# Kernel optimization log

Measured on AMD Instinct MI355X. Metric: run time of the kernel, lower is better.

The kernel has to match this reference:

```python
import jax, jax.numpy as jnp
import numpy as np
from functools import partial

N_NODES = 100000
N_REL = 3
N_EDGES = 200000
IN_F = 128
HID_F = 128
OUT_F = 128
N_QUERY = 4096


def _graph_conv(x, es, ed, W, b, n_nodes):
    """DGL GraphConv with norm='both': D_dst^{-1/2} A D_src^{-1/2} X W + b.
    es/ed: [E] int edge endpoints, x: [N, d_in], W: [d_in, d_out], b: [d_out]."""
    ones = jnp.ones(es.shape[0], dtype=x.dtype)
    out_deg = jnp.clip(jax.ops.segment_sum(ones, es, num_segments=n_nodes), 1.0)
    in_deg = jnp.clip(jax.ops.segment_sum(ones, ed, num_segments=n_nodes), 1.0)
    # transform first (dense GEMM), then gather -> scatter-add over dst
    y = (x * jax.lax.rsqrt(out_deg)[:, None]) @ W          # [N, d_out]
    msg = y[es]                                            # [E, d_out] gather
    agg = jax.ops.segment_sum(msg, ed, num_segments=n_nodes)  # [N, d_out]
    return agg * jax.lax.rsqrt(in_deg)[:, None] + b


def _hetero_layer(x, e_src, e_dst, W, b, n_nodes):
    # HeteroGraphConv(aggregate='sum'): sum per-relation GraphConv outputs.
    out = _graph_conv(x, e_src[0], e_dst[0], W[0], b[0], n_nodes)
    for r in range(1, e_src.shape[0]):
        out = out + _graph_conv(x, e_src[r], e_dst[r], W[r], b[r], n_nodes)
    return out


def setup_inputs() -> dict:
    key = jax.random.key(0)
    ks = jax.random.split(key, 9)
    s = 1.0 / np.sqrt(IN_F)
    return {
        "emb": jax.random.normal(ks[0], (N_NODES, IN_F), jnp.float32),
        "W1": jax.random.normal(ks[1], (N_REL, IN_F, HID_F), jnp.float32) * s,
        "b1": jnp.zeros((N_REL, HID_F), jnp.float32),
        "W2": jax.random.normal(ks[2], (N_REL, HID_F, OUT_F), jnp.float32) * s,
        "b2": jnp.zeros((N_REL, OUT_F), jnp.float32),
        "e_src": jax.random.randint(ks[3], (N_REL, N_EDGES), 0, N_NODES, jnp.int32),
        "e_dst": jax.random.randint(ks[4], (N_REL, N_EDGES), 0, N_NODES, jnp.int32),
        "src": jax.random.randint(ks[5], (N_QUERY,), 0, N_NODES, jnp.int32),
        "dst": jax.random.randint(ks[6], (N_QUERY,), 0, N_NODES, jnp.int32),
    }


def reference(emb, W1, b1, W2, b2, e_src, e_dst, src, dst):
    n = emb.shape[0]
    h = jnp.tanh(_hetero_layer(emb, e_src, e_dst, W1, b1, n))
    h = jnp.tanh(_hetero_layer(h, e_src, e_dst, W2, b2, n))
    return (h[src], h[dst])
```

## Files before the change

### kernel.cpp

```cpp
#include <hip/hip_runtime.h>
#include <stdint.h>

#define NN 100000
#define NREL 3
#define NE 200000
#define F 128
#define NQ 4096

#define NBUCK (NREL * NN)
#define NCB ((NBUCK + 255) / 256)
#define CH_BLOCKS 512
#define CH_CHUNK ((NREL * NE + CH_BLOCKS - 1) / CH_BLOCKS)

#define WCVT_N (2 * NREL * F * F)
#define A1 (WCVT_N + 256)
#define A2 (A1 + NN * F / 8)
#define A3 (A2 + 2 * NQ)
#define A4 (A3 + NN)
#define PREP_N (A4 + 1)

typedef float fx4 __attribute__((ext_vector_type(4)));
typedef unsigned short u16x8 __attribute__((ext_vector_type(8)));
typedef __bf16 bf16x8 __attribute__((ext_vector_type(8)));

__device__ __forceinline__ unsigned short f2bf(float f) {
  uint32_t u = __builtin_bit_cast(uint32_t, f);
  uint32_t r = u + 0x7FFFu + ((u >> 16) & 1u);
  return (unsigned short)(r >> 16);
}
__device__ __forceinline__ float bf2f(unsigned short u) {
  return __builtin_bit_cast(float, (uint32_t)u << 16);
}
__device__ __forceinline__ int rel_of(int i) {
  return (i >= 2 * NE) ? 2 : (i >= NE ? 1 : 0);
}

__global__ void prep_kernel(const float* __restrict__ W1, const float* __restrict__ W2,
                            const float* __restrict__ b1, const float* __restrict__ b2,
                            const float* __restrict__ emb,
                            const int* __restrict__ qsrc, const int* __restrict__ qdst,
                            unsigned short* __restrict__ Wtb, float* __restrict__ bsum,
                            unsigned short* __restrict__ xb,
                            int* __restrict__ qnode, int* __restrict__ mark,
                            int* __restrict__ cursor) {
  int i = blockIdx.x * blockDim.x + threadIdx.x;
  if (i < WCVT_N) {
    int l = i / (NREL * F * F);
    int rem = i % (NREL * F * F);
    int r = rem / (F * F);
    int nk = rem % (F * F);
    int n = nk >> 7, k = nk & 127;
    const float* W = l ? W2 : W1;
    Wtb[i] = f2bf(W[r * F * F + k * F + n]);
  } else if (i < A1) {
    int t = i - WCVT_N;
    int l = t >> 7, f = t & 127;
    const float* b = l ? b2 : b1;
    bsum[l * F + f] = b[f] + b[F + f] + b[2 * F + f];
  } else if (i < A2) {
    int j = i - A1;
    const float* p = emb + (size_t)j * 8;
    unsigned short tmp[8];
#pragma unroll
    for (int e = 0; e < 8; ++e) tmp[e] = f2bf(p[e]);
    *reinterpret_cast<u16x8*>(xb + (size_t)j * 8) = *reinterpret_cast<u16x8*>(tmp);
  } else if (i < A3) {
    int m = i - A2;
    qnode[m] = (m < NQ) ? qsrc[m] : qdst[m - NQ];
  } else if (i < A4) {
    mark[i - A3] = 0;
  } else if (i < PREP_N) {
    *cursor = 0;
  }
}

__global__ __launch_bounds__(256) void coarseHH_kernel(const int* __restrict__ es,
                                                       const int* __restrict__ ed,
                                                       int* __restrict__ Hd,
                                                       int* __restrict__ Hs) {
  __shared__ int hd[NCB], hs[NCB];
  int t = threadIdx.x, blk = blockIdx.x;
  for (int j = t; j < NCB; j += 256) { hd[j] = 0; hs[j] = 0; }
  __syncthreads();
  int lo = blk * CH_CHUNK;
  int hi = min(lo + CH_CHUNK, NREL * NE);
  for (int i = lo + t; i < hi; i += 256) {
    int r = rel_of(i);
    atomicAdd(&hd[(r * NN + ed[i]) >> 8], 1);
    atomicAdd(&hs[(r * NN + es[i]) >> 8], 1);
  }
  __syncthreads();
  for (int j = t; j < NCB; j += 256) {
    Hd[j * CH_BLOCKS + blk] = hd[j];
    Hs[j * CH_BLOCKS + blk] = hs[j];
  }
}

__global__ __launch_bounds__(256) void hsum_kernel(const int* __restrict__ Hd,
                                                   const int* __restrict__ Hs,
                                                   int* __restrict__ chist_d,
                                                   int* __restrict__ chist_s) {
  int t = threadIdx.x, lane = t & 63;
  int ws = blockIdx.x * 4 + (t >> 6);
  if (ws >= 2 * NCB) return;
  const int* H = (ws < NCB) ? Hd : Hs;
  int bin = (ws < NCB) ? ws : ws - NCB;
  int s = 0;
#pragma unroll
  for (int k = 0; k < 8; ++k) s += H[bin * CH_BLOCKS + lane * 8 + k];
#pragma unroll
  for (int d = 1; d < 64; d <<= 1) s += __shfl_xor(s, d);
  if (lane == 0) {
    if (ws < NCB) chist_d[bin] = s; else chist_s[bin] = s;
  }
}

__global__ __launch_bounds__(256) void cscan_kernel(const int* __restrict__ chist_d,
                                                    const int* __restrict__ chist_s,
                                                    int* __restrict__ cstart_d,
                                                    int* __restrict__ cstart_s) {
  const int* chist = blockIdx.x ? chist_s : chist_d;
  int* cstart = blockIdx.x ? cstart_s : cstart_d;
  int t = threadIdx.x, lane = t & 63, w = t >> 6;
  int v[5];
  int s = 0;
#pragma unroll
  for (int k = 0; k < 5; ++k) {
    int i = t * 5 + k;
    v[k] = (i < NCB) ? chist[i] : 0;
    s += v[k];
  }
  int sc = s;
#pragma unroll
  for (int d = 1; d < 64; d <<= 1) {
    int o = __shfl_up(sc, d);
    if (lane >= d) sc += o;
  }
  __shared__ int wt[4];
  if (lane == 63) wt[w] = sc;
  __syncthreads();
  int woff = 0;
#pragma unroll
  for (int ww = 0; ww < 3; ++ww) woff += (ww < w) ? wt[ww] : 0;
  int excl = woff + sc - s;
#pragma unroll
  for (int k = 0; k < 5; ++k) {
    int i = t * 5 + k;
    if (i < NCB) { cstart[i] = excl; excl += v[k]; }
  }
}

__global__ __launch_bounds__(256) void hbase_kernel(const int* __restrict__ Hd,
                                                    const int* __restrict__ Hs,
                                                    const int* __restrict__ cstart_d,
                                                    const int* __restrict__ cstart_s,
                                                    int* __restrict__ Hbase_d,
                                                    int* __restrict__ Hbase_s) {
  const int* H = blockIdx.y ? Hs : Hd;
  const int* cstart = blockIdx.y ? cstart_s : cstart_d;
  int* Hbase = blockIdx.y ? Hbase_s : Hbase_d;
  int t = threadIdx.x, lane = t & 63;
  int bin = blockIdx.x * 4 + (t >> 6);
  int v[8];
  int s = 0;
#pragma unroll
  for (int k = 0; k < 8; ++k) {
    v[k] = H[bin * CH_BLOCKS + lane * 8 + k];
    s += v[k];
  }
  int sc = s;
#pragma unroll
  for (int d = 1; d < 64; d <<= 1) {
    int o = __shfl_up(sc, d);
    if (lane >= d) sc += o;
  }
  int run = cstart[bin] + sc - s;
#pragma unroll
  for (int k = 0; k < 8; ++k) {
    Hbase[bin * CH_BLOCKS + lane * 8 + k] = run;
    run += v[k];
  }
}

__global__ __launch_bounds__(256) void cscatter_kernel(const int* __restrict__ es,
                                                       const int* __restrict__ ed,
                                                       const int* __restrict__ Hbase_d,
                                                       const int* __restrict__ Hbase_s,
                                                       int* __restrict__ etmp_d,
                                                       int* __restrict__ etmp_s) {
  __shared__ int cur_d[NCB], cur_s[NCB];
  int t = threadIdx.x, blk = blockIdx.x;
  for (int j = t; j < NCB; j += 256) {
    cur_d[j] = Hbase_d[j * CH_BLOCKS + blk];
    cur_s[j] = Hbase_s[j * CH_BLOCKS + blk];
  }
  __syncthreads();
  int lo = blk * CH_CHUNK;
  int hi = min(lo + CH_CHUNK, NREL * NE);
  for (int i = lo + t; i < hi; i += 256) {
    int r = rel_of(i);
    int s = es[i], d = ed[i];
    int bd = r * NN + d;
    int pos = atomicAdd(&cur_d[bd >> 8], 1);
    etmp_d[pos] = (s << 8) | (bd & 255);
    int bs = r * NN + s;
    int pos_s = atomicAdd(&cur_s[bs >> 8], 1);
    etmp_s[pos_s] = bs & 255;
  }
}

__global__ __launch_bounds__(256) void srccount_kernel(const int* __restrict__ etmp_s,
                                                       const int* __restrict__ cstart_s,
                                                       const int* __restrict__ chist_s,
                                                       int* __restrict__ cnt_src) {
  const int cb = blockIdx.x;
  const int t = threadIdx.x;
  const int cs = cstart_s[cb], cc = chist_s[cb];
  __shared__ int fcnt[256];
  fcnt[t] = 0;
  __syncthreads();
  for (int i = t; i < cc; i += 256) atomicAdd(&fcnt[etmp_s[cs + i]], 1);
  __syncthreads();
  int b = cb * 256 + t;
  if (b < NBUCK) cnt_src[b] = fcnt[t];
}

__global__ __launch_bounds__(256) void fine_kernel(const int* __restrict__ etmp,
                                                   const int* __restrict__ cstart,
                                                   const int* __restrict__ chist,
                                                   const int* __restrict__ cnt_src,
                                                   int2* __restrict__ scb,
                                                   int2* __restrict__ epay) {
  const int cb = blockIdx.x;
  const int t = threadIdx.x, lane = t & 63, w = t >> 6;
  const int cs = cstart[cb], cc = chist[cb];
  __shared__ int fcnt[256], fexcl[256], fcur[256];
  fcnt[t] = 0;
  fcur[t] = 0;
  __syncthreads();
  for (int i = t; i < cc; i += 256) atomicAdd(&fcnt[etmp[cs + i] & 255], 1);
  __syncthreads();
  int val = fcnt[t];
  int sc = val;
#pragma unroll
  for (int d = 1; d < 64; d <<= 1) {
    int o = __shfl_up(sc, d);
    if (lane >= d) sc += o;
  }
  __shared__ int wt[4];
  if (lane == 63) wt[w] = sc;
  __syncthreads();
  int woff = 0;
#pragma unroll
  for (int ww = 0; ww < 3; ++ww) woff += (ww < w) ? wt[ww] : 0;
  fexcl[t] = woff + sc - val;
  int b = cb * 256 + t;
  if (b < NBUCK) scb[b] = make_int2(cs + fexcl[t], val);
  __syncthreads();
  for (int i = t; i < cc; i += 256) {
    int e = etmp[cs + i];
    int f = e & 255;
    int src = ((unsigned)e) >> 8;
    int r = (cb * 256 + f) / NN;
    float wgt = rsqrtf((float)cnt_src[r * NN + src]) * rsqrtf((float)fcnt[f]);
    int pos = cs + fexcl[f] + atomicAdd(&fcur[f], 1);
    epay[pos] = make_int2(src, __builtin_bit_cast(int, wgt));
  }
}

__global__ void mark_kernel(const int* __restrict__ qnode, const int2* __restrict__ scb,
                            const int2* __restrict__ epay, int* __restrict__ mark) {
  int m = blockIdx.x * blockDim.x + threadIdx.x;
  if (m >= 2 * NQ) return;
  int n = qnode[m];
#pragma unroll
  for (int r = 0; r < NREL; ++r) {
    int2 meta = scb[r * NN + n];
    for (int i = 0; i < meta.y; ++i) mark[epay[meta.x + i].x] = 1;
  }
}

__global__ __launch_bounds__(256) void compact_kernel(const int* __restrict__ mark,
                                                      int* __restrict__ list,
                                                      int* __restrict__ cursor) {
  int t = threadIdx.x, lane = t & 63, w = t >> 6;
  int base = blockIdx.x * 1024 + t * 4;
  int loc[4];
  int cnt = 0;
#pragma unroll
  for (int k = 0; k < 4; ++k) {
    int i = base + k;
    if (i < NN && mark[i]) { loc[cnt] = i; ++cnt; }
  }
  int sc = cnt;
#pragma unroll
  for (int d = 1; d < 64; d <<= 1) {
    int o = __shfl_up(sc, d);
    if (lane >= d) sc += o;
  }
  int texcl = sc - cnt;
  __shared__ int wt[4];
  __shared__ int bb;
  if (lane == 63) wt[w] = sc;
  __syncthreads();
  if (t == 0) {
    int tot = wt[0] + wt[1] + wt[2] + wt[3];
    bb = atomicAdd(cursor, tot);
    int a = 0;
#pragma unroll
    for (int ww = 0; ww < 4; ++ww) { int c = wt[ww]; wt[ww] = a; a += c; }
  }
  __syncthreads();
  int p = bb + wt[w] + texcl;
  for (int k = 0; k < cnt; ++k) list[p + k] = loc[k];
}

__global__ __launch_bounds__(256) void aggz_kernel(const unsigned short* __restrict__ X,
                                                   const int2* __restrict__ scb,
                                                   const int2* __restrict__ epay,
                                                   const int* __restrict__ nmap,
                                                   const int* __restrict__ cntp,
                                                   unsigned short* __restrict__ Z,
                                                   int Mcap, int Ms) {
  const int count = cntp ? *cntp : Mcap;
  const int r = blockIdx.y;
  const int t = threadIdx.x;
  const int lane = t & 63;
  const int m = blockIdx.x * 16 + (t >> 6) * 4 + (lane >> 4);
  const int j = lane & 15;
  if (m >= count) return;
  int n = nmap ? nmap[m] : m;
  int2 meta = scb[r * NN + n];
  const int2* ep = epay + meta.x;
  const int c = meta.y;

  float ps[8];
#pragma unroll
  for (int k = 0; k < 8; ++k) ps[k] = 0.f;

  int i = 0;
  for (; i + 2 <= c; i += 2) {
    int2 p0 = ep[i], p1 = ep[i + 1];
    float w0 = __builtin_bit_cast(float, p0.y);
    float w1 = __builtin_bit_cast(float, p1.y);
    u16x8 v0 = *reinterpret_cast<const u16x8*>(X + ((size_t)p0.x << 7) + j * 8);
    u16x8 v1 = *reinterpret_cast<const u16x8*>(X + ((size_t)p1.x << 7) + j * 8);
#pragma unroll
    for (int k = 0; k < 8; ++k)
      ps[k] = fmaf(bf2f(v1[k]), w1, fmaf(bf2f(v0[k]), w0, ps[k]));
  }
  if (i < c) {
    int2 p0 = ep[i];
    float w0 = __builtin_bit_cast(float, p0.y);
    u16x8 v0 = *reinterpret_cast<const u16x8*>(X + ((size_t)p0.x << 7) + j * 8);
#pragma unroll
    for (int k = 0; k < 8; ++k) ps[k] = fmaf(bf2f(v0[k]), w0, ps[k]);
  }

  unsigned short tmp[8];
#pragma unroll
  for (int k = 0; k < 8; ++k) tmp[k] = f2bf(ps[k]);
  *reinterpret_cast<u16x8*>(Z + (((size_t)r * Ms + m) << 7) + j * 8) =
      *reinterpret_cast<u16x8*>(tmp);
}

#define GBM 128
__global__ __launch_bounds__(512) void gemmp_kernel(const unsigned short* __restrict__ Z,
                                                    const unsigned short* __restrict__ Wt3,
                                                    const float* __restrict__ bsum,
                                                    const int* __restrict__ omap,
                                                    const int* __restrict__ cntp,
                                                    void* __restrict__ outp,
                                                    int M, int Ms, int out_f32) {
  const int count = cntp ? *cntp : M;
  const int m0 = blockIdx.x * GBM;
  if (m0 >= count) return;
  __shared__ unsigned short Abuf[2][GBM * F];
  const int t = threadIdx.x;
  const int lane = t & 63, w = t >> 6;
  const int wm = w >> 2, wn = w & 3;
  const int r0 = lane & 15, kq = lane >> 4;

  fx4 acc[4][2];
#pragma unroll
  for (int mt = 0; mt < 4; ++mt)
#pragma unroll
    for (int nt = 0; nt < 2; ++nt) acc[mt][nt] = (fx4){0.f, 0.f, 0.f, 0.f};

  {
    const unsigned short* Zr = Z + (size_t)m0 * F;
#pragma unroll
    for (int i = 0; i < 4; ++i) {
      int slot = i * 512 + t;
      int row = slot >> 4, s = slot & 15;
      __builtin_amdgcn_global_load_lds(
          (const __attribute__((address_space(1))) uint32_t*)(
              Zr + ((size_t)row << 7) + ((s ^ (row & 7)) << 3)),
          (__attribute__((address_space(3))) uint32_t*)&Abuf[0][slot * 8], 16, 0, 0);
    }
  }
  __syncthreads();

  int cur = 0;
  for (int r = 0; r < NREL; ++r) {
    bf16x8 bfrag[2][4];
    const unsigned short* Wt = Wt3 + (size_t)r * F * F;
#pragma unroll
    for (int nt = 0; nt < 2; ++nt)
#pragma unroll
      for (int kb = 0; kb < 4; ++kb)
        bfrag[nt][kb] = __builtin_bit_cast(bf16x8,
            *reinterpret_cast<const u16x8*>(
                Wt + (wn * 32 + nt * 16 + r0) * F + (4 * kb + kq) * 8));

    if (r + 1 < NREL) {
      const unsigned short* Zr = Z + ((size_t)(r + 1) * Ms + m0) * F;
#pragma unroll
      for (int i = 0; i < 4; ++i) {
        int slot = i * 512 + t;
        int row = slot >> 4, s = slot & 15;
        __builtin_amdgcn_global_load_lds(
            (const __attribute__((address_space(1))) uint32_t*)(
                Zr + ((size_t)row << 7) + ((s ^ (row & 7)) << 3)),
            (__attribute__((address_space(3))) uint32_t*)&Abuf[cur ^ 1][slot * 8],
            16, 0, 0);
      }
    }

#pragma unroll
    for (int kb = 0; kb < 4; ++kb) {
      const int cs = ((kb * 4 + kq) ^ (r0 & 7)) * 8;
      bf16x8 a[4];
#pragma unroll
      for (int mt = 0; mt < 4; ++mt)
        a[mt] = __builtin_bit_cast(bf16x8,
            *reinterpret_cast<const u16x8*>(&Abuf[cur][(wm * 64 + mt * 16 + r0) * F + cs]));
#pragma unroll
      for (int mt = 0; mt < 4; ++mt)
#pragma unroll
        for (int nt = 0; nt < 2; ++nt)
          acc[mt][nt] = __builtin_amdgcn_mfma_f32_16x16x32_bf16(a[mt], bfrag[nt][kb],
                                                                acc[mt][nt], 0, 0, 0);
    }

    __syncthreads();
    cur ^= 1;
  }

#pragma unroll
  for (int mt = 0; mt < 4; ++mt) {
    const int rbase = m0 + wm * 64 + mt * 16 + kq * 4;
#pragma unroll
    for (int nt = 0; nt < 2; ++nt) {
      int col = wn * 32 + nt * 16 + r0;
      float bb = bsum[col];
#pragma unroll
      for (int reg = 0; reg < 4; ++reg) {
        int gm = rbase + reg;
        if (gm < count) {
          float v = tanhf(acc[mt][nt][reg] + bb);
          if (omap) {
            ((unsigned short*)outp)[(size_t)omap[gm] * F + col] = f2bf(v);
          } else if (out_f32) {
            ((float*)outp)[(size_t)gm * F + col] = v;
          } else {
            ((unsigned short*)outp)[(size_t)gm * F + col] = f2bf(v);
          }
        }
      }
    }
  }
}

extern "C" void kernel_launch(void* const* d_in, const int* in_sizes, int n_in,
                              void* d_out, int out_size, void* d_ws, size_t ws_size,
                              hipStream_t stream) {
  const float* emb = (const float*)d_in[0];
  const float* W1  = (const float*)d_in[1];
  const float* b1  = (const float*)d_in[2];
  const float* W2  = (const float*)d_in[3];
  const float* b2  = (const float*)d_in[4];
  const int* e_src = (const int*)d_in[5];
  const int* e_dst = (const int*)d_in[6];
  const int* qsrc  = (const int*)d_in[7];
  const int* qdst  = (const int*)d_in[8];
  float* out = (float*)d_out;

  const int MS1 = ((NN + GBM - 1) / GBM) * GBM;
  const int MQ  = 2 * NQ;

  char* p = (char*)d_ws;
  size_t off = 0;
  auto take = [&](size_t n) { void* q = p + off; off = (off + n + 255) & ~(size_t)255; return q; };
  int* cnt_src  = (int*)take((size_t)NREL * NN * 4);
  int* chist_d  = (int*)take((size_t)NCB * 4);
  int* chist_s  = (int*)take((size_t)NCB * 4);
  int* cstart_d = (int*)take((size_t)NCB * 4);
  int* cstart_s = (int*)take((size_t)NCB * 4);
  int* Hd       = (int*)take((size_t)NCB * CH_BLOCKS * 4);
  int* Hs       = (int*)take((size_t)NCB * CH_BLOCKS * 4);
  int* Hbase_d  = (int*)take((size_t)NCB * CH_BLOCKS * 4);
  int* Hbase_s  = (int*)take((size_t)NCB * CH_BLOCKS * 4);
  int* etmp_d   = (int*)take((size_t)NREL * NE * 4);
  int* etmp_s   = (int*)take((size_t)NREL * NE * 4);
  int2* scb     = (int2*)take((size_t)NBUCK * 8);
  int2* epay    = (int2*)take((size_t)NREL * NE * 8);
  unsigned short* Wtb = (unsigned short*)take(2ull * NREL * F * F * 2);
  float* bsum   = (float*)take(2ull * F * 4);
  int* qnode    = (int*)take((size_t)MQ * 4);
  int* mark     = (int*)take((size_t)NN * 4);
  int* list     = (int*)take((size_t)NN * 4 + 4);
  int* cursor   = (int*)take(4);
  unsigned short* Xb  = (unsigned short*)take((size_t)NN * F * 2);
  unsigned short* Xb2 = (unsigned short*)take((size_t)NN * F * 2);
  unsigned short* Z   = (unsigned short*)take((size_t)NREL * MS1 * F * 2);

  prep_kernel<<<(PREP_N + 255) / 256, 256, 0, stream>>>(
      W1, W2, b1, b2, emb, qsrc, qdst, Wtb, bsum, Xb, qnode, mark, cursor);
  coarseHH_kernel<<<CH_BLOCKS, 256, 0, stream>>>(e_src, e_dst, Hd, Hs);
  hsum_kernel<<<(2 * NCB + 3) / 4, 256, 0, stream>>>(Hd, Hs, chist_d, chist_s);
  cscan_kernel<<<2, 256, 0, stream>>>(chist_d, chist_s, cstart_d, cstart_s);
  {
    dim3 hb(NCB / 4, 2);
    hbase_kernel<<<hb, 256, 0, stream>>>(Hd, Hs, cstart_d, cstart_s, Hbase_d, Hbase_s);
  }
  cscatter_kernel<<<CH_BLOCKS, 256, 0, stream>>>(e_src, e_dst, Hbase_d, Hbase_s,
                                                 etmp_d, etmp_s);
  srccount_kernel<<<NCB, 256, 0, stream>>>(etmp_s, cstart_s, chist_s, cnt_src);
  fine_kernel<<<NCB, 256, 0, stream>>>(etmp_d, cstart_d, chist_d, cnt_src, scb, epay);
  mark_kernel<<<(MQ + 255) / 256, 256, 0, stream>>>(qnode, scb, epay, mark);
  compact_kernel<<<(NN + 1023) / 1024, 256, 0, stream>>>(mark, list, cursor);

  dim3 ag1((NN + 15) / 16, NREL);
  aggz_kernel<<<ag1, 256, 0, stream>>>(Xb, scb, epay, list, cursor, Z, NN, MS1);
  gemmp_kernel<<<MS1 / GBM, 512, 0, stream>>>(Z, Wtb, bsum, list, cursor, Xb2, MS1, MS1, 0);

  dim3 ag2((MQ + 15) / 16, NREL);
  aggz_kernel<<<ag2, 256, 0, stream>>>(Xb2, scb, epay, qnode, nullptr, Z, MQ, MQ);
  gemmp_kernel<<<MQ / GBM, 512, 0, stream>>>(
      Z, Wtb + (size_t)NREL * F * F, bsum + F, nullptr, nullptr, out, MQ, MQ, 1);
}
```

Before: 153.2 us.

## Merge prep with coarse histogram and fold query-neighbor marking into fine sort

Merges the prep kernel and the coarse histogram kernel into one launch, using block index ranges to split the two jobs. Query nodes are flagged during the histogram-sum kernel. The fine bucketing kernel then marks the sources of edges whose destination is a query node, which removes the separate serial mark kernel. This cuts two launches and the per-thread serial walk over edge lists, at the cost of an extra flag array and an extra flag read per edge in the fine kernel. hsum_kernel launches only about 586 blocks, enough to cover all 8192 query slots.

```diff
diff --git a/kernel.cpp b/kernel.cpp
--- a/kernel.cpp
+++ b/kernel.cpp
@@ -17,7 +17,9 @@
 #define A2 (A1 + NN * F / 8)
 #define A3 (A2 + 2 * NQ)
 #define A4 (A3 + NN)
-#define PREP_N (A4 + 1)
+#define A5 (A4 + NN)
+#define PREP_N (A5 + 1)
+#define PREP_BLKS ((PREP_N + 255) / 256)
 
 typedef float fx4 __attribute__((ext_vector_type(4)));
 typedef unsigned short u16x8 __attribute__((ext_vector_type(8)));
@@ -35,15 +37,38 @@
   return (i >= 2 * NE) ? 2 : (i >= NE ? 1 : 0);
 }
 
-__global__ void prep_kernel(const float* __restrict__ W1, const float* __restrict__ W2,
-                            const float* __restrict__ b1, const float* __restrict__ b2,
-                            const float* __restrict__ emb,
-                            const int* __restrict__ qsrc, const int* __restrict__ qdst,
-                            unsigned short* __restrict__ Wtb, float* __restrict__ bsum,
-                            unsigned short* __restrict__ xb,
-                            int* __restrict__ qnode, int* __restrict__ mark,
-                            int* __restrict__ cursor) {
-  int i = blockIdx.x * blockDim.x + threadIdx.x;
+__global__ __launch_bounds__(256) void prepch_kernel(
+    const float* __restrict__ W1, const float* __restrict__ W2,
+    const float* __restrict__ b1, const float* __restrict__ b2,
+    const float* __restrict__ emb,
+    const int* __restrict__ qsrc, const int* __restrict__ qdst,
+    const int* __restrict__ es, const int* __restrict__ ed,
+    unsigned short* __restrict__ Wtb, float* __restrict__ bsum,
+    unsigned short* __restrict__ xb,
+    int* __restrict__ qnode, int* __restrict__ mark, int* __restrict__ qflag,
+    int* __restrict__ cursor,
+    int* __restrict__ Hd, int* __restrict__ Hs) {
+  __shared__ int hd[NCB], hs[NCB];
+  int t = threadIdx.x;
+  if (blockIdx.x >= PREP_BLKS) {
+    int blk = blockIdx.x - PREP_BLKS;
+    for (int j = t; j < NCB; j += 256) { hd[j] = 0; hs[j] = 0; }
+    __syncthreads();
+    int lo = blk * CH_CHUNK;
+    int hi = min(lo + CH_CHUNK, NREL * NE);
+    for (int i = lo + t; i < hi; i += 256) {
+      int r = rel_of(i);
+      atomicAdd(&hd[(r * NN + ed[i]) >> 8], 1);
+      atomicAdd(&hs[(r * NN + es[i]) >> 8], 1);
+    }
+    __syncthreads();
+    for (int j = t; j < NCB; j += 256) {
+      Hd[j * CH_BLOCKS + blk] = hd[j];
+      Hs[j * CH_BLOCKS + blk] = hs[j];
+    }
+    return;
+  }
+  int i = blockIdx.x * blockDim.x + t;
   if (i < WCVT_N) {
     int l = i / (NREL * F * F);
     int rem = i % (NREL * F * F);
@@ -53,8 +78,8 @@
     const float* W = l ? W2 : W1;
     Wtb[i] = f2bf(W[r * F * F + k * F + n]);
   } else if (i < A1) {
-    int t = i - WCVT_N;
-    int l = t >> 7, f = t & 127;
+    int tt = i - WCVT_N;
+    int l = tt >> 7, f = tt & 127;
     const float* b = l ? b2 : b1;
     bsum[l * F + f] = b[f] + b[F + f] + b[2 * F + f];
   } else if (i < A2) {
@@ -69,38 +94,22 @@
     qnode[m] = (m < NQ) ? qsrc[m] : qdst[m - NQ];
   } else if (i < A4) {
     mark[i - A3] = 0;
+  } else if (i < A5) {
+    qflag[i - A4] = 0;
   } else if (i < PREP_N) {
     *cursor = 0;
   }
 }
 
-__global__ __launch_bounds__(256) void coarseHH_kernel(const int* __restrict__ es,
-                                                       const int* __restrict__ ed,
-                                                       int* __restrict__ Hd,
-                                                       int* __restrict__ Hs) {
-  __shared__ int hd[NCB], hs[NCB];
-  int t = threadIdx.x, blk = blockIdx.x;
-  for (int j = t; j < NCB; j += 256) { hd[j] = 0; hs[j] = 0; }
-  __syncthreads();
-  int lo = blk * CH_CHUNK;
-  int hi = min(lo + CH_CHUNK, NREL * NE);
-  for (int i = lo + t; i < hi; i += 256) {
-    int r = rel_of(i);
-    atomicAdd(&hd[(r * NN + ed[i]) >> 8], 1);
-    atomicAdd(&hs[(r * NN + es[i]) >> 8], 1);
-  }
-  __syncthreads();
-  for (int j = t; j < NCB; j += 256) {
-    Hd[j * CH_BLOCKS + blk] = hd[j];
-    Hs[j * CH_BLOCKS + blk] = hs[j];
-  }
-}
-
 __global__ __launch_bounds__(256) void hsum_kernel(const int* __restrict__ Hd,
                                                    const int* __restrict__ Hs,
+                                                   const int* __restrict__ qnode,
                                                    int* __restrict__ chist_d,
-                                                   int* __restrict__ chist_s) {
+                                                   int* __restrict__ chist_s,
+                                                   int* __restrict__ qflag) {
   int t = threadIdx.x, lane = t & 63;
+  int q = blockIdx.x * 256 + t;
+  if (q < 2 * NQ) qflag[qnode[q]] = 1;
   int ws = blockIdx.x * 4 + (t >> 6);
   if (ws >= 2 * NCB) return;
   const int* H = (ws < NCB) ? Hd : Hs;
@@ -229,8 +238,10 @@
                                                    const int* __restrict__ cstart,
                                                    const int* __restrict__ chist,
                                                    const int* __restrict__ cnt_src,
+                                                   const int* __restrict__ qflag,
                                                    int2* __restrict__ scb,
-                                                   int2* __restrict__ epay) {
+                                                   int2* __restrict__ epay,
+                                                   int* __restrict__ mark) {
   const int cb = blockIdx.x;
   const int t = threadIdx.x, lane = t & 63, w = t >> 6;
   const int cs = cstart[cb], cc = chist[cb];
@@ -261,22 +272,13 @@
     int e = etmp[cs + i];
     int f = e & 255;
     int src = ((unsigned)e) >> 8;
-    int r = (cb * 256 + f) / NN;
+    int fine = cb * 256 + f;
+    int r = fine / NN;
+    int dst = fine - r * NN;
     float wgt = rsqrtf((float)cnt_src[r * NN + src]) * rsqrtf((float)fcnt[f]);
     int pos = cs + fexcl[f] + atomicAdd(&fcur[f], 1);
     epay[pos] = make_int2(src, __builtin_bit_cast(int, wgt));
-  }
-}
-
-__global__ void mark_kernel(const int* __restrict__ qnode, const int2* __restrict__ scb,
-                            const int2* __restrict__ epay, int* __restrict__ mark) {
-  int m = blockIdx.x * blockDim.x + threadIdx.x;
-  if (m >= 2 * NQ) return;
-  int n = qnode[m];
-#pragma unroll
-  for (int r = 0; r < NREL; ++r) {
-    int2 meta = scb[r * NN + n];
-    for (int i = 0; i < meta.y; ++i) mark[epay[meta.x + i].x] = 1;
+    if (qflag[dst]) mark[src] = 1;
   }
 }
 
@@ -509,16 +511,18 @@
   float* bsum   = (float*)take(2ull * F * 4);
   int* qnode    = (int*)take((size_t)MQ * 4);
   int* mark     = (int*)take((size_t)NN * 4);
+  int* qflag    = (int*)take((size_t)NN * 4);
   int* list     = (int*)take((size_t)NN * 4 + 4);
   int* cursor   = (int*)take(4);
   unsigned short* Xb  = (unsigned short*)take((size_t)NN * F * 2);
   unsigned short* Xb2 = (unsigned short*)take((size_t)NN * F * 2);
   unsigned short* Z   = (unsigned short*)take((size_t)NREL * MS1 * F * 2);
 
-  prep_kernel<<<(PREP_N + 255) / 256, 256, 0, stream>>>(
-      W1, W2, b1, b2, emb, qsrc, qdst, Wtb, bsum, Xb, qnode, mark, cursor);
-  coarseHH_kernel<<<CH_BLOCKS, 256, 0, stream>>>(e_src, e_dst, Hd, Hs);
-  hsum_kernel<<<(2 * NCB + 3) / 4, 256, 0, stream>>>(Hd, Hs, chist_d, chist_s);
+  prepch_kernel<<<PREP_BLKS + CH_BLOCKS, 256, 0, stream>>>(
+      W1, W2, b1, b2, emb, qsrc, qdst, e_src, e_dst,
+      Wtb, bsum, Xb, qnode, mark, qflag, cursor, Hd, Hs);
+  hsum_kernel<<<(2 * NCB + 3) / 4, 256, 0, stream>>>(Hd, Hs, qnode,
+                                                     chist_d, chist_s, qflag);
   cscan_kernel<<<2, 256, 0, stream>>>(chist_d, chist_s, cstart_d, cstart_s);
   {
     dim3 hb(NCB / 4, 2);
@@ -527,8 +531,8 @@
   cscatter_kernel<<<CH_BLOCKS, 256, 0, stream>>>(e_src, e_dst, Hbase_d, Hbase_s,
                                                  etmp_d, etmp_s);
   srccount_kernel<<<NCB, 256, 0, stream>>>(etmp_s, cstart_s, chist_s, cnt_src);
-  fine_kernel<<<NCB, 256, 0, stream>>>(etmp_d, cstart_d, chist_d, cnt_src, scb, epay);
-  mark_kernel<<<(MQ + 255) / 256, 256, 0, stream>>>(qnode, scb, epay, mark);
+  fine_kernel<<<NCB, 256, 0, stream>>>(etmp_d, cstart_d, chist_d, cnt_src, qflag,
+                                       scb, epay, mark);
   compact_kernel<<<(NN + 1023) / 1024, 256, 0, stream>>>(mark, list, cursor);
 
   dim3 ag1((NN + 15) / 16, NREL);
```

Measured after the change: 148.9 us. 1.03x faster.
